# Optimization experiments

Measured on AMD Instinct MI355X. Metric: run time of the kernel, lower is better.

## Reference

```python
import jax, jax.numpy as jnp
import numpy as np
import math

HIDDEN = 128

def setup_inputs() -> dict:
    key = jax.random.key(0)
    k1, k2, k3 = jax.random.split(key, 3)
    X = jax.random.normal(k1, (4, 4096, HIDDEN), dtype=jnp.float32)
    # nn.Linear(hidden, 3*hidden): weight [3H, H], bias [3H]
    bound = 1.0 / math.sqrt(HIDDEN)
    W = jax.random.uniform(k2, (3 * HIDDEN, HIDDEN), minval=-bound, maxval=bound, dtype=jnp.float32)
    b = jax.random.uniform(k3, (3 * HIDDEN,), minval=-bound, maxval=bound, dtype=jnp.float32)
    return {"X": X, "W": W, "b": b}

def reference(X, W, b):
    H = X.shape[-1]
    # fused QKV projection: X @ W^T + b -> [B, S, 3H]
    qkv = jnp.einsum('bsh,oh->bso', X, W) + b
    Q, K, V = jnp.split(qkv, 3, axis=-1)
    # scaled dot-product attention (single head)
    scores = jnp.einsum('bqh,bkh->bqk', Q, K) / jnp.sqrt(jnp.asarray(H, X.dtype))
    weights = jax.nn.softmax(scores, axis=-1)
    return jnp.einsum('bqk,bkh->bqh', weights, V)
```

## Files before the change

### kernel.cpp

```cpp
#include <hip/hip_runtime.h>
#include <hip/hip_fp16.h>

typedef _Float16 f16;
typedef __attribute__((ext_vector_type(8))) _Float16 f16x8;
typedef __attribute__((ext_vector_type(4))) float f32x4;
typedef __attribute__((ext_vector_type(16))) float f32x16;
typedef __attribute__((ext_vector_type(4))) unsigned int u32x4;
typedef __attribute__((ext_vector_type(2))) unsigned int u32x2;

#define BB 4
#define SS 4096
#define HH 128
#define SC2 0.12752462157076558f
#define M2  5.7707801635558535f

union H2U { __half2 h; unsigned int u; };
union VU { u32x4 v; unsigned short s[8]; };
union F8U { u32x4 u; f16x8 h; };

__global__ __launch_bounds__(256) void wcvt(const float* __restrict__ W,
                                            f16* __restrict__ Wh)
{
    const int idx = (blockIdx.x * 256 + threadIdx.x) * 4;
    float4 v = *(const float4*)(W + idx);
    H2U h0, h1;
    h0.h = __floats2half2_rn(v.x, v.y);
    h1.h = __floats2half2_rn(v.z, v.w);
    u32x2 pk; pk.x = h0.u; pk.y = h1.u;
    *(u32x2*)(Wh + idx) = pk;
}

__global__ __launch_bounds__(256, 2) void qkv_gemm(
    const float* __restrict__ X, const f16* __restrict__ Wh,
    const float* __restrict__ bias, f16* __restrict__ Qh,
    f16* __restrict__ Kh, f16* __restrict__ Vh)
{
    const int bid = blockIdx.x;
    const int t = threadIdx.x;
    const int w = t >> 6, lane = t & 63;
    const int c = lane & 15, quad = lane >> 4;
    const int rbase = bid * 64;

    f16x8 wf[6][4];
#pragma unroll
    for (int mt = 0; mt < 6; ++mt) {
        const f16* wr = Wh + (size_t)(w * 96 + mt * 16 + c) * HH + quad * 8;
#pragma unroll
        for (int kc = 0; kc < 4; ++kc)
            wf[mt][kc] = *(const f16x8*)(wr + kc * 32);
    }
    float4 bb[6];
#pragma unroll
    for (int mt = 0; mt < 6; ++mt)
        bb[mt] = *(const float4*)&bias[w * 96 + mt * 16 + quad * 4];

#pragma unroll
    for (int nt = 0; nt < 4; ++nt) {
        f16x8 xf[4];
        const float* xr = X + (size_t)(rbase + nt * 16 + c) * HH + quad * 8;
#pragma unroll
        for (int kc = 0; kc < 4; ++kc) {
            float4 a = *(const float4*)(xr + kc * 32);
            float4 b = *(const float4*)(xr + kc * 32 + 4);
            H2U u0, u1, u2, u3;
            u0.h = __floats2half2_rn(a.x, a.y);
            u1.h = __floats2half2_rn(a.z, a.w);
            u2.h = __floats2half2_rn(b.x, b.y);
            u3.h = __floats2half2_rn(b.z, b.w);
            F8U pk; pk.u.x = u0.u; pk.u.y = u1.u; pk.u.z = u2.u; pk.u.w = u3.u;
            xf[kc] = pk.h;
        }
        f32x4 acc[6];
#pragma unroll
        for (int mt = 0; mt < 6; ++mt) acc[mt] = (f32x4)0.f;
#pragma unroll
        for (int kc = 0; kc < 4; ++kc)
#pragma unroll
            for (int mt = 0; mt < 6; ++mt)
                acc[mt] = __builtin_amdgcn_mfma_f32_16x16x32_f16(wf[mt][kc], xf[kc], acc[mt], 0, 0, 0);

        const int xrow = rbase + nt * 16 + c;
#pragma unroll
        for (int mt = 0; mt < 6; ++mt) {
            const int gcol = w * 96 + mt * 16;
            const int seg = gcol >> 7;
            const int cc = (gcol & 127) + quad * 4;
            f16* dst = (seg == 0) ? Qh : (seg == 1) ? Kh : Vh;
            H2U h0, h1;
            h0.h = __floats2half2_rn(acc[mt][0] + bb[mt].x, acc[mt][1] + bb[mt].y);
            h1.h = __floats2half2_rn(acc[mt][2] + bb[mt].z, acc[mt][3] + bb[mt].w);
            u32x2 pk; pk.x = h0.u; pk.y = h1.u;
            *(u32x2*)(dst + (size_t)xrow * HH + cc) = pk;
        }
    }
}

#define BM 128
#define BN 64
#define LK 136
#define LV 72

__global__ __launch_bounds__(256, 2) void attn_mfma(
    const f16* __restrict__ Qh, const f16* __restrict__ Kh,
    const f16* __restrict__ Vh, float* __restrict__ out,
    float* __restrict__ Opart, float* __restrict__ l_arr, int nsplit)
{
    __shared__ f16 sK[BN * LK];
    __shared__ f16 sVt[HH * LV];

    const int bid = blockIdx.x;
    const int split = bid >> 7;
    const int inner = bid & 127;
    const int batch = inner & 3;
    const int qtile = inner >> 2;
    const int t = threadIdx.x;
    const int w = t >> 6, lane = t & 63;
    const int l31 = lane & 31, hi = lane >> 5;

    const int s0 = (64 * split) / nsplit;
    const int s1 = (64 * (split + 1)) / nsplit;
    const int nst = s1 - s0;
    const int kstart = s0 * BN;

    const f16* Qb = Qh + (size_t)batch * SS * HH;
    const f16* Kb = Kh + (size_t)batch * SS * HH;
    const f16* Vb = Vh + (size_t)batch * SS * HH;
    const int qbase = qtile * BM + w * 32;

    f16x8 qfr[8];
#pragma unroll
    for (int ks = 0; ks < 8; ++ks)
        qfr[ks] = *(const f16x8*)(Qb + (size_t)(qbase + l31) * HH + ks * 16 + hi * 8);

    const int kr = t >> 2, q4 = t & 3;
    const f16* kgp = Kb + (size_t)(kstart + kr) * HH + q4 * 32;
    f16* ksp = sK + kr * LK + q4 * 32;
    const int vkp = t & 31, vhq = t >> 5;
    const f16* vgp = Vb + (size_t)(kstart + 2 * vkp) * HH + vhq * 16;

    u32x4 kbuf[4], vb0[2], vb1[2];
#pragma unroll
    for (int i = 0; i < 4; ++i) kbuf[i] = *(const u32x4*)(kgp + i * 8);
#pragma unroll
    for (int i = 0; i < 2; ++i) {
        vb0[i] = *(const u32x4*)(vgp + i * 8);
        vb1[i] = *(const u32x4*)(vgp + HH + i * 8);
    }

    f32x16 oacc[4];
#pragma unroll
    for (int dt = 0; dt < 4; ++dt) oacc[dt] = (f32x16)0.f;
    f32x16 lacc = (f32x16)0.f;
    const f16x8 ones = {1, 1, 1, 1, 1, 1, 1, 1};

    for (int st = 0; st < nst; ++st) {
        __syncthreads();
#pragma unroll
        for (int i = 0; i < 4; ++i) *(u32x4*)(ksp + i * 8) = kbuf[i];
        {
            VU a0, a1, b0, b1;
            a0.v = vb0[0]; a1.v = vb0[1]; b0.v = vb1[0]; b1.v = vb1[1];
#pragma unroll
            for (int d = 0; d < 8; ++d) {
                unsigned int pk = (unsigned int)a0.s[d] | ((unsigned int)b0.s[d] << 16);
                *(unsigned int*)&sVt[(vhq * 16 + d) * LV + 2 * vkp] = pk;
            }
#pragma unroll
            for (int d = 0; d < 8; ++d) {
                unsigned int pk = (unsigned int)a1.s[d] | ((unsigned int)b1.s[d] << 16);
                *(unsigned int*)&sVt[(vhq * 16 + 8 + d) * LV + 2 * vkp] = pk;
            }
        }
        __syncthreads();
        if (st + 1 < nst) {
            const f16* kg = kgp + (size_t)(st + 1) * BN * HH;
#pragma unroll
            for (int i = 0; i < 4; ++i) kbuf[i] = *(const u32x4*)(kg + i * 8);
            const f16* vg = vgp + (size_t)(st + 1) * BN * HH;
#pragma unroll
            for (int i = 0; i < 2; ++i) {
                vb0[i] = *(const u32x4*)(vg + i * 8);
                vb1[i] = *(const u32x4*)(vg + HH + i * 8);
            }
        }

#pragma unroll
        for (int kt = 0; kt < 2; ++kt) {
            f32x16 sacc = (f32x16)0.f;
            __builtin_amdgcn_s_setprio(1);
#pragma unroll
            for (int ks = 0; ks < 8; ++ks) {
                f16x8 kf = *(const f16x8*)&sK[(kt * 32 + l31) * LK + ks * 16 + hi * 8];
                sacc = __builtin_amdgcn_mfma_f32_32x32x16_f16(kf, qfr[ks], sacc, 0, 0, 0);
            }
            __builtin_amdgcn_s_setprio(0);
            float p[16];
#pragma unroll
            for (int r = 0; r < 16; ++r) p[r] = exp2f(sacc[r] * SC2 - M2);
            f16x8 pf[2];
#pragma unroll
            for (int ks2 = 0; ks2 < 2; ++ks2) {
                const int b = ks2 * 8;
                H2U u0, u1, u2, u3;
                u0.h = __floats2half2_rn(p[b + 0], p[b + 1]);
                u1.h = __floats2half2_rn(p[b + 2], p[b + 3]);
                u2.h = __floats2half2_rn(p[b + 4], p[b + 5]);
                u3.h = __floats2half2_rn(p[b + 6], p[b + 7]);
                auto s0v = __builtin_amdgcn_permlane32_swap(u0.u, u2.u, false, false);
                auto s1v = __builtin_amdgcn_permlane32_swap(u1.u, u3.u, false, false);
                F8U pu;
                pu.u.x = s0v[0]; pu.u.y = s1v[0]; pu.u.z = s0v[1]; pu.u.w = s1v[1];
                pf[ks2] = pu.h;
            }
            __builtin_amdgcn_s_setprio(1);
#pragma unroll
            for (int ks2 = 0; ks2 < 2; ++ks2) {
                lacc = __builtin_amdgcn_mfma_f32_32x32x16_f16(pf[ks2], ones, lacc, 0, 0, 0);
#pragma unroll
                for (int dt = 0; dt < 4; ++dt) {
                    f16x8 vf = *(const f16x8*)&sVt[(dt * 32 + l31) * LV + kt * 32 + ks2 * 16 + hi * 8];
                    oacc[dt] = __builtin_amdgcn_mfma_f32_32x32x16_f16(pf[ks2], vf, oacc[dt], 0, 0, 0);
                }
            }
            __builtin_amdgcn_s_setprio(0);
        }
    }

    float* Ob = (split == 0) ? out : (Opart + (size_t)(split - 1) * BB * SS * HH);
    float* ob = Ob + (size_t)(batch * SS + qbase) * HH;
    if (nsplit == 1) {
#pragma unroll
        for (int r = 0; r < 16; ++r) {
            const int qr = (r & 3) + 8 * (r >> 2) + 4 * hi;
            const float inv = 1.f / lacc[r];
#pragma unroll
            for (int dt = 0; dt < 4; ++dt)
                ob[(size_t)qr * HH + dt * 32 + l31] = oacc[dt][r] * inv;
        }
    } else {
#pragma unroll
        for (int r = 0; r < 16; ++r) {
            const int qr = (r & 3) + 8 * (r >> 2) + 4 * hi;
#pragma unroll
            for (int dt = 0; dt < 4; ++dt)
                ob[(size_t)qr * HH + dt * 32 + l31] = oacc[dt][r];
        }
        if (l31 == 0) {
#pragma unroll
            for (int r = 0; r < 16; ++r) {
                const int qr = (r & 3) + 8 * (r >> 2) + 4 * hi;
                l_arr[((size_t)split * BB + batch) * SS + qbase + qr] = lacc[r];
            }
        }
    }
}

__global__ __launch_bounds__(256) void attn_merge(
    float* __restrict__ out, const float* __restrict__ Opart,
    const float* __restrict__ l_arr, int nsplit)
{
    const int idx = blockIdx.x * 256 + threadIdx.x;
    const int chunk = idx & 31;
    const int q = (idx >> 5) & (SS - 1);
    const int b = idx >> 17;
    float L = 0.f;
    for (int s = 0; s < nsplit; ++s)
        L += l_arr[((size_t)s * BB + b) * SS + q];
    float4 a = *(const float4*)(out + ((size_t)b * SS + q) * HH + chunk * 4);
    for (int s = 1; s < nsplit; ++s) {
        const float* Op = Opart + (size_t)(s - 1) * BB * SS * HH;
        float4 o = *(const float4*)(Op + ((size_t)b * SS + q) * HH + chunk * 4);
        a.x += o.x; a.y += o.y; a.z += o.z; a.w += o.w;
    }
    const float inv = 1.f / L;
    a.x *= inv; a.y *= inv; a.z *= inv; a.w *= inv;
    *(float4*)(out + ((size_t)b * SS + q) * HH + chunk * 4) = a;
}

extern "C" void kernel_launch(void* const* d_in, const int* in_sizes, int n_in,
                              void* d_out, int out_size, void* d_ws, size_t ws_size,
                              hipStream_t stream) {
    const float* X = (const float*)d_in[0];
    const float* W = (const float*)d_in[1];
    const float* bias = (const float*)d_in[2];
    float* out = (float*)d_out;

    char* ws = (char*)d_ws;
    const size_t qkv_bytes = (size_t)3 * BB * SS * HH * sizeof(f16);
    const size_t wh_bytes  = (size_t)384 * HH * sizeof(f16);
    const size_t o_bytes   = (size_t)BB * SS * HH * sizeof(float);
    const size_t l_bytes   = (size_t)BB * SS * sizeof(float);

    int S = 1;
    for (int cand = 8; cand >= 2; cand -= 2) {
        if (ws_size >= qkv_bytes + wh_bytes + (size_t)(cand - 1) * o_bytes + (size_t)cand * l_bytes) {
            S = cand; break;
        }
    }

    f16* Qh = (f16*)ws;
    f16* Kh = Qh + (size_t)BB * SS * HH;
    f16* Vh = Kh + (size_t)BB * SS * HH;
    f16* Wh = (f16*)(ws + qkv_bytes);
    float* Opart = (float*)(ws + qkv_bytes + wh_bytes);
    float* l_arr = (float*)(ws + qkv_bytes + wh_bytes + (size_t)(S - 1) * o_bytes);

    wcvt<<<48, 256, 0, stream>>>(W, Wh);
    qkv_gemm<<<256, 256, 0, stream>>>(X, Wh, bias, Qh, Kh, Vh);
    attn_mfma<<<128 * S, 256, 0, stream>>>(Qh, Kh, Vh, out, Opart, l_arr, S);
    if (S > 1)
        attn_merge<<<BB * SS * (HH / 4) / 256, 256, 0, stream>>>(out, Opart, l_arr, S);
}
```

Measured before the change: 138.1 us.

## Software-pipeline QK and PV MFMAs across key subtiles; cap KV split at 4

Restructures the inner attention loop so the QK^T MFMAs for the second 32-key subtile are issued before the exp/pack and PV MFMAs of the first subtile. This lets softmax VALU work overlap with matrix-core work. Each QK chain is split into two independent accumulators to shorten MFMA dependency chains, at the cost of more registers. The KV split count is also capped at 4 instead of 8, so fewer partial outputs need to be written and merged, with less grid parallelism in exchange.

New measurement: 130.9 us. 5.3% less time.

```diff
diff --git a/kernel.cpp b/kernel.cpp
--- a/kernel.cpp
+++ b/kernel.cpp
@@ -100,6 +100,19 @@
 #define LK 136
 #define LV 72
 
+__device__ __forceinline__ f16x8 packP(const float* p) {
+    H2U u0, u1, u2, u3;
+    u0.h = __floats2half2_rn(p[0], p[1]);
+    u1.h = __floats2half2_rn(p[2], p[3]);
+    u2.h = __floats2half2_rn(p[4], p[5]);
+    u3.h = __floats2half2_rn(p[6], p[7]);
+    auto s0v = __builtin_amdgcn_permlane32_swap(u0.u, u2.u, false, false);
+    auto s1v = __builtin_amdgcn_permlane32_swap(u1.u, u3.u, false, false);
+    F8U pu;
+    pu.u.x = s0v[0]; pu.u.y = s1v[0]; pu.u.z = s0v[1]; pu.u.w = s1v[1];
+    return pu.h;
+}
+
 __global__ __launch_bounds__(256, 2) void attn_mfma(
     const f16* __restrict__ Qh, const f16* __restrict__ Kh,
     const f16* __restrict__ Vh, float* __restrict__ out,
@@ -184,46 +197,70 @@
             }
         }
 
-#pragma unroll
-        for (int kt = 0; kt < 2; ++kt) {
-            f32x16 sacc = (f32x16)0.f;
-            __builtin_amdgcn_s_setprio(1);
-#pragma unroll
-            for (int ks = 0; ks < 8; ++ks) {
-                f16x8 kf = *(const f16x8*)&sK[(kt * 32 + l31) * LK + ks * 16 + hi * 8];
-                sacc = __builtin_amdgcn_mfma_f32_32x32x16_f16(kf, qfr[ks], sacc, 0, 0, 0);
-            }
-            __builtin_amdgcn_s_setprio(0);
-            float p[16];
-#pragma unroll
-            for (int r = 0; r < 16; ++r) p[r] = exp2f(sacc[r] * SC2 - M2);
-            f16x8 pf[2];
-#pragma unroll
-            for (int ks2 = 0; ks2 < 2; ++ks2) {
-                const int b = ks2 * 8;
-                H2U u0, u1, u2, u3;
-                u0.h = __floats2half2_rn(p[b + 0], p[b + 1]);
-                u1.h = __floats2half2_rn(p[b + 2], p[b + 3]);
-                u2.h = __floats2half2_rn(p[b + 4], p[b + 5]);
-                u3.h = __floats2half2_rn(p[b + 6], p[b + 7]);
-                auto s0v = __builtin_amdgcn_permlane32_swap(u0.u, u2.u, false, false);
-                auto s1v = __builtin_amdgcn_permlane32_swap(u1.u, u3.u, false, false);
-                F8U pu;
-                pu.u.x = s0v[0]; pu.u.y = s1v[0]; pu.u.z = s0v[1]; pu.u.w = s1v[1];
-                pf[ks2] = pu.h;
-            }
-            __builtin_amdgcn_s_setprio(1);
-#pragma unroll
-            for (int ks2 = 0; ks2 < 2; ++ks2) {
-                lacc = __builtin_amdgcn_mfma_f32_32x32x16_f16(pf[ks2], ones, lacc, 0, 0, 0);
-#pragma unroll
-                for (int dt = 0; dt < 4; ++dt) {
-                    f16x8 vf = *(const f16x8*)&sVt[(dt * 32 + l31) * LV + kt * 32 + ks2 * 16 + hi * 8];
-                    oacc[dt] = __builtin_amdgcn_mfma_f32_32x32x16_f16(pf[ks2], vf, oacc[dt], 0, 0, 0);
-                }
-            }
-            __builtin_amdgcn_s_setprio(0);
-        }
+        f32x16 s0a = (f32x16)0.f, s0b = (f32x16)0.f;
+        __builtin_amdgcn_s_setprio(1);
+#pragma unroll
+        for (int ks = 0; ks < 8; ks += 2) {
+            f16x8 kfa = *(const f16x8*)&sK[(l31) * LK + ks * 16 + hi * 8];
+            f16x8 kfb = *(const f16x8*)&sK[(l31) * LK + (ks + 1) * 16 + hi * 8];
+            s0a = __builtin_amdgcn_mfma_f32_32x32x16_f16(kfa, qfr[ks], s0a, 0, 0, 0);
+            s0b = __builtin_amdgcn_mfma_f32_32x32x16_f16(kfb, qfr[ks + 1], s0b, 0, 0, 0);
+        }
+        __builtin_amdgcn_s_setprio(0);
+
+        float p0[16];
+#pragma unroll
+        for (int r = 0; r < 16; ++r)
+            p0[r] = exp2f((s0a[r] + s0b[r]) * SC2 - M2);
+
+        f32x16 s1a = (f32x16)0.f, s1b = (f32x16)0.f;
+        __builtin_amdgcn_s_setprio(1);
+#pragma unroll
+        for (int ks = 0; ks < 8; ks += 2) {
+            f16x8 kfa = *(const f16x8*)&sK[(32 + l31) * LK + ks * 16 + hi * 8];
+            f16x8 kfb = *(const f16x8*)&sK[(32 + l31) * LK + (ks + 1) * 16 + hi * 8];
+            s1a = __builtin_amdgcn_mfma_f32_32x32x16_f16(kfa, qfr[ks], s1a, 0, 0, 0);
+            s1b = __builtin_amdgcn_mfma_f32_32x32x16_f16(kfb, qfr[ks + 1], s1b, 0, 0, 0);
+        }
+        __builtin_amdgcn_s_setprio(0);
+
+        f16x8 pf00 = packP(&p0[0]);
+        f16x8 pf01 = packP(&p0[8]);
+        __builtin_amdgcn_s_setprio(1);
+        lacc = __builtin_amdgcn_mfma_f32_32x32x16_f16(pf00, ones, lacc, 0, 0, 0);
+#pragma unroll
+        for (int dt = 0; dt < 4; ++dt) {
+            f16x8 vf = *(const f16x8*)&sVt[(dt * 32 + l31) * LV + 0 * 32 + 0 * 16 + hi * 8];
+            oacc[dt] = __builtin_amdgcn_mfma_f32_32x32x16_f16(pf00, vf, oacc[dt], 0, 0, 0);
+        }
+        lacc = __builtin_amdgcn_mfma_f32_32x32x16_f16(pf01, ones, lacc, 0, 0, 0);
+#pragma unroll
+        for (int dt = 0; dt < 4; ++dt) {
+            f16x8 vf = *(const f16x8*)&sVt[(dt * 32 + l31) * LV + 0 * 32 + 1 * 16 + hi * 8];
+            oacc[dt] = __builtin_amdgcn_mfma_f32_32x32x16_f16(pf01, vf, oacc[dt], 0, 0, 0);
+        }
+        __builtin_amdgcn_s_setprio(0);
+
+        float p1[16];
+#pragma unroll
+        for (int r = 0; r < 16; ++r)
+            p1[r] = exp2f((s1a[r] + s1b[r]) * SC2 - M2);
+        f16x8 pf10 = packP(&p1[0]);
+        f16x8 pf11 = packP(&p1[8]);
+        __builtin_amdgcn_s_setprio(1);
+        lacc = __builtin_amdgcn_mfma_f32_32x32x16_f16(pf10, ones, lacc, 0, 0, 0);
+#pragma unroll
+        for (int dt = 0; dt < 4; ++dt) {
+            f16x8 vf = *(const f16x8*)&sVt[(dt * 32 + l31) * LV + 1 * 32 + 0 * 16 + hi * 8];
+            oacc[dt] = __builtin_amdgcn_mfma_f32_32x32x16_f16(pf10, vf, oacc[dt], 0, 0, 0);
+        }
+        lacc = __builtin_amdgcn_mfma_f32_32x32x16_f16(pf11, ones, lacc, 0, 0, 0);
+#pragma unroll
+        for (int dt = 0; dt < 4; ++dt) {
+            f16x8 vf = *(const f16x8*)&sVt[(dt * 32 + l31) * LV + 1 * 32 + 1 * 16 + hi * 8];
+            oacc[dt] = __builtin_amdgcn_mfma_f32_32x32x16_f16(pf11, vf, oacc[dt], 0, 0, 0);
+        }
+        __builtin_amdgcn_s_setprio(0);
     }
 
     float* Ob = (split == 0) ? out : (Opart + (size_t)(split - 1) * BB * SS * HH);
@@ -292,7 +329,7 @@
     const size_t l_bytes   = (size_t)BB * SS * sizeof(float);
 
     int S = 1;
-    for (int cand = 8; cand >= 2; cand -= 2) {
+    for (int cand = 4; cand >= 2; --cand) {
         if (ws_size >= qkv_bytes + wh_bytes + (size_t)(cand - 1) * o_bytes + (size_t)cand * l_bytes) {
             S = cand; break;
         }
```

## Stream K tiles into double-buffered swizzled LDS via direct global-to-LDS loads

Applied to the files above, without the earlier changes.

K tiles are now loaded with global_load_lds straight into a double-buffered, XOR-swizzled shared buffer, replacing the register staging and padded layout. The row-sum of probabilities is computed with scalar adds plus a cross-lane shuffle instead of an extra MFMA against a ones vector. Launch bounds rise to 3 blocks per CU, and the split-K candidate list drops 8 in favour of 6, 4 and 2. The aim is fewer VGPRs, less LDS store traffic and less MFMA work. The risks are the added LDS footprint, the missing explicit wait for the async K loads before the sync, and register spilling at the higher occupancy target.

Result: slower. 168.0 us (+21.6%).

```diff
diff --git a/kernel.cpp b/kernel.cpp
--- a/kernel.cpp
+++ b/kernel.cpp
@@ -97,15 +97,14 @@
 
 #define BM 128
 #define BN 64
-#define LK 136
 #define LV 72
 
-__global__ __launch_bounds__(256, 2) void attn_mfma(
+__global__ __launch_bounds__(256, 3) void attn_mfma(
     const f16* __restrict__ Qh, const f16* __restrict__ Kh,
     const f16* __restrict__ Vh, float* __restrict__ out,
     float* __restrict__ Opart, float* __restrict__ l_arr, int nsplit)
 {
-    __shared__ f16 sK[BN * LK];
+    __shared__ f16 sK[2][BN * HH];
     __shared__ f16 sVt[HH * LV];
 
     const int bid = blockIdx.x;
@@ -132,56 +131,73 @@
     for (int ks = 0; ks < 8; ++ks)
         qfr[ks] = *(const f16x8*)(Qb + (size_t)(qbase + l31) * HH + ks * 16 + hi * 8);
 
-    const int kr = t >> 2, q4 = t & 3;
-    const f16* kgp = Kb + (size_t)(kstart + kr) * HH + q4 * 32;
-    f16* ksp = sK + kr * LK + q4 * 32;
+    const int l4 = lane >> 4, b16 = lane & 15;
+    int ksrcoff[4];
+#pragma unroll
+    for (int i = 0; i < 4; ++i) {
+        const int row = (w << 4) + (i << 2) + l4;
+        const int bs = b16 ^ (row & 7);
+        ksrcoff[i] = row * HH + bs * 8;
+    }
+    const int swz = (l31 & 7) << 3;
+
+#define ISSUE_K(stp, nb)                                                      \
+    {                                                                         \
+        const f16* kg_ = Kb + (size_t)(kstart + (stp) * BN) * HH;             \
+        _Pragma("unroll")                                                     \
+        for (int i = 0; i < 4; ++i)                                           \
+            __builtin_amdgcn_global_load_lds(                                 \
+                (const __attribute__((address_space(1))) void*)(kg_ + ksrcoff[i]), \
+                (__attribute__((address_space(3))) void*)&sK[nb][((w << 4) + (i << 2)) * HH], \
+                16, 0, 0);                                                    \
+    }
+
     const int vkp = t & 31, vhq = t >> 5;
     const f16* vgp = Vb + (size_t)(kstart + 2 * vkp) * HH + vhq * 16;
-
-    u32x4 kbuf[4], vb0[2], vb1[2];
-#pragma unroll
-    for (int i = 0; i < 4; ++i) kbuf[i] = *(const u32x4*)(kgp + i * 8);
-#pragma unroll
-    for (int i = 0; i < 2; ++i) {
-        vb0[i] = *(const u32x4*)(vgp + i * 8);
-        vb1[i] = *(const u32x4*)(vgp + HH + i * 8);
-    }
+    u32x4 vb0[2], vb1[2];
+
+#define LOAD_V(stp)                                                           \
+    {                                                                         \
+        const f16* vg_ = vgp + (size_t)(stp) * BN * HH;                       \
+        _Pragma("unroll")                                                     \
+        for (int i = 0; i < 2; ++i) {                                         \
+            vb0[i] = *(const u32x4*)(vg_ + i * 8);                            \
+            vb1[i] = *(const u32x4*)(vg_ + HH + i * 8);                       \
+        }                                                                     \
+    }
+
+#define WRITE_V()                                                             \
+    {                                                                         \
+        VU a0, a1, b0, b1;                                                    \
+        a0.v = vb0[0]; a1.v = vb0[1]; b0.v = vb1[0]; b1.v = vb1[1];           \
+        _Pragma("unroll")                                                     \
+        for (int d = 0; d < 8; ++d) {                                         \
+            unsigned int pk = (unsigned int)a0.s[d] | ((unsigned int)b0.s[d] << 16); \
+            *(unsigned int*)&sVt[(vhq * 16 + d) * LV + 2 * vkp] = pk;         \
+        }                                                                     \
+        _Pragma("unroll")                                                     \
+        for (int d = 0; d < 8; ++d) {                                         \
+            unsigned int pk = (unsigned int)a1.s[d] | ((unsigned int)b1.s[d] << 16); \
+            *(unsigned int*)&sVt[(vhq * 16 + 8 + d) * LV + 2 * vkp] = pk;     \
+        }                                                                     \
+    }
+
+    ISSUE_K(0, 0);
+    LOAD_V(0);
 
     f32x16 oacc[4];
 #pragma unroll
     for (int dt = 0; dt < 4; ++dt) oacc[dt] = (f32x16)0.f;
-    f32x16 lacc = (f32x16)0.f;
-    const f16x8 ones = {1, 1, 1, 1, 1, 1, 1, 1};
+    float lsum = 0.f;
 
     for (int st = 0; st < nst; ++st) {
+        const int cur = st & 1;
         __syncthreads();
-#pragma unroll
-        for (int i = 0; i < 4; ++i) *(u32x4*)(ksp + i * 8) = kbuf[i];
-        {
-            VU a0, a1, b0, b1;
-            a0.v = vb0[0]; a1.v = vb0[1]; b0.v = vb1[0]; b1.v = vb1[1];
-#pragma unroll
-            for (int d = 0; d < 8; ++d) {
-                unsigned int pk = (unsigned int)a0.s[d] | ((unsigned int)b0.s[d] << 16);
-                *(unsigned int*)&sVt[(vhq * 16 + d) * LV + 2 * vkp] = pk;
-            }
-#pragma unroll
-            for (int d = 0; d < 8; ++d) {
-                unsigned int pk = (unsigned int)a1.s[d] | ((unsigned int)b1.s[d] << 16);
-                *(unsigned int*)&sVt[(vhq * 16 + 8 + d) * LV + 2 * vkp] = pk;
-            }
-        }
+        WRITE_V();
         __syncthreads();
         if (st + 1 < nst) {
-            const f16* kg = kgp + (size_t)(st + 1) * BN * HH;
-#pragma unroll
-            for (int i = 0; i < 4; ++i) kbuf[i] = *(const u32x4*)(kg + i * 8);
-            const f16* vg = vgp + (size_t)(st + 1) * BN * HH;
-#pragma unroll
-            for (int i = 0; i < 2; ++i) {
-                vb0[i] = *(const u32x4*)(vg + i * 8);
-                vb1[i] = *(const u32x4*)(vg + HH + i * 8);
-            }
+            ISSUE_K(st + 1, cur ^ 1);
+            LOAD_V(st + 1);
         }
 
 #pragma unroll
@@ -190,13 +206,20 @@
             __builtin_amdgcn_s_setprio(1);
 #pragma unroll
             for (int ks = 0; ks < 8; ++ks) {
-                f16x8 kf = *(const f16x8*)&sK[(kt * 32 + l31) * LK + ks * 16 + hi * 8];
+                f16x8 kf = *(const f16x8*)&sK[cur][(kt * 32 + l31) * HH + ((ks * 16 + hi * 8) ^ swz)];
                 sacc = __builtin_amdgcn_mfma_f32_32x32x16_f16(kf, qfr[ks], sacc, 0, 0, 0);
             }
             __builtin_amdgcn_s_setprio(0);
             float p[16];
 #pragma unroll
             for (int r = 0; r < 16; ++r) p[r] = exp2f(sacc[r] * SC2 - M2);
+            {
+                float s01 = (p[0] + p[1]) + (p[2] + p[3]);
+                float s23 = (p[4] + p[5]) + (p[6] + p[7]);
+                float s45 = (p[8] + p[9]) + (p[10] + p[11]);
+                float s67 = (p[12] + p[13]) + (p[14] + p[15]);
+                lsum += (s01 + s23) + (s45 + s67);
+            }
             f16x8 pf[2];
 #pragma unroll
             for (int ks2 = 0; ks2 < 2; ++ks2) {
@@ -215,7 +238,6 @@
             __builtin_amdgcn_s_setprio(1);
 #pragma unroll
             for (int ks2 = 0; ks2 < 2; ++ks2) {
-                lacc = __builtin_amdgcn_mfma_f32_32x32x16_f16(pf[ks2], ones, lacc, 0, 0, 0);
 #pragma unroll
                 for (int dt = 0; dt < 4; ++dt) {
                     f16x8 vf = *(const f16x8*)&sVt[(dt * 32 + l31) * LV + kt * 32 + ks2 * 16 + hi * 8];
@@ -226,16 +248,18 @@
         }
     }
 
+    const float ltot = lsum + __shfl_xor(lsum, 32, 64);
     float* Ob = (split == 0) ? out : (Opart + (size_t)(split - 1) * BB * SS * HH);
     float* ob = Ob + (size_t)(batch * SS + qbase) * HH;
     if (nsplit == 1) {
+        const float inv = 1.f / ltot;
 #pragma unroll
         for (int r = 0; r < 16; ++r) {
             const int qr = (r & 3) + 8 * (r >> 2) + 4 * hi;
-            const float inv = 1.f / lacc[r];
+            const float invr = __shfl(inv, qr, 64);
 #pragma unroll
             for (int dt = 0; dt < 4; ++dt)
-                ob[(size_t)qr * HH + dt * 32 + l31] = oacc[dt][r] * inv;
+                ob[(size_t)qr * HH + dt * 32 + l31] = oacc[dt][r] * invr;
         }
     } else {
 #pragma unroll
@@ -245,14 +269,12 @@
             for (int dt = 0; dt < 4; ++dt)
                 ob[(size_t)qr * HH + dt * 32 + l31] = oacc[dt][r];
         }
-        if (l31 == 0) {
-#pragma unroll
-            for (int r = 0; r < 16; ++r) {
-                const int qr = (r & 3) + 8 * (r >> 2) + 4 * hi;
-                l_arr[((size_t)split * BB + batch) * SS + qbase + qr] = lacc[r];
-            }
-        }
-    }
+        if (hi == 0)
+            l_arr[((size_t)split * BB + batch) * SS + qbase + l31] = ltot;
+    }
+#undef ISSUE_K
+#undef LOAD_V
+#undef WRITE_V
 }
 
 __global__ __launch_bounds__(256) void attn_merge(
@@ -291,8 +313,10 @@
     const size_t o_bytes   = (size_t)BB * SS * HH * sizeof(float);
     const size_t l_bytes   = (size_t)BB * SS * sizeof(float);
 
+    const int cands[3] = {6, 4, 2};
     int S = 1;
-    for (int cand = 8; cand >= 2; cand -= 2) {
+    for (int ci = 0; ci < 3; ++ci) {
+        const int cand = cands[ci];
         if (ws_size >= qkv_bytes + wh_bytes + (size_t)(cand - 1) * o_bytes + (size_t)cand * l_bytes) {
             S = cand; break;
         }
```
